# Optimization experiments

Hardware: AMD Instinct MI355X
Metric: run time of the kernel (lower is better)

## Reference

```python
import jax, jax.numpy as jnp
import numpy as np

B, H, W, C = 32, 128, 128, 64
MX, MY = 32, 32  # modes_x, modes_y


def setup_inputs() -> dict:
    key = jax.random.key(0)
    k1, k2, k3, k4 = jax.random.split(key, 4)
    # glorot-ish scales for the spectral and conv weights
    wscale = (2.0 / (C + C)) ** 0.5
    return {
        "x": jax.random.normal(k1, (B, H, W, C), dtype=jnp.float32),
        "w_real": jax.random.normal(k2, (MX, MY, C, C), dtype=jnp.float32) * wscale,
        "w_imag": jax.random.normal(k3, (MX, MY, C, C), dtype=jnp.float32) * wscale,
        "conv_w": jax.random.normal(k4, (C, C), dtype=jnp.float32) * wscale,
        "conv_b": jnp.zeros((C,), dtype=jnp.float32),
    }


def reference(x, w_real, w_imag, conv_w, conv_b):
    # Complex spectral mixing weights [MX, MY, Cin, Cout]
    weights = jax.lax.complex(w_real, w_imag)
    # tf.signal.fft2d transforms the innermost TWO axes of [B,H,W,C],
    # i.e. axes (W, C); jnp.fft.fft2 default axes=(-2,-1) matches exactly.
    x_ft = jnp.fft.fft2(x.astype(jnp.complex64))           # [B,H,W,C] complex64
    # Mode truncation on axes (H, W), as in the original code.
    x_ft_trunc = x_ft[:, :MX, :MY, :]                      # [B,MX,MY,C]
    # Complex channel-mixing einsum over the low modes.
    x_ft_proc = jnp.einsum('bxyi,xyio->bxyo', x_ft_trunc, weights)  # [B,MX,MY,C]
    # Zero-pad back to the full grid on (H, W).
    x_ft_padded = jnp.pad(x_ft_proc,
                          ((0, 0), (0, H - MX), (0, W - MY), (0, 0)))
    # IFFT again over innermost two axes (W, C), take real part.
    x_spec = jnp.real(jnp.fft.ifft2(x_ft_padded))          # [B,H,W,C] float32
    # 1x1 conv (pointwise channel mix) + bias on the raw input.
    x_local = jnp.einsum('bhwi,io->bhwo', x, conv_w) + conv_b
    return jax.nn.relu(x_spec + x_local)
```

## Files before the change

kernel.cpp:

```cpp
#include <hip/hip_runtime.h>

typedef __attribute__((ext_vector_type(8))) short short8;
typedef __attribute__((ext_vector_type(4))) float f32x4;
typedef unsigned short ushort_t;

#define MFMA(a, b, c) __builtin_amdgcn_mfma_f32_16x16x32_bf16((a), (b), (c), 0, 0, 0)

constexpr int NB = 32, NHt = 128, NWd = 128, NC = 64, MX = 32;
constexpr float TWO_PI = 6.28318530717958647692f;

constexpr size_t TAB_T1 = 0;
constexpr size_t TAB_T2 = 16384;
constexpr size_t TAB_T3 = 32768;
constexpr size_t TAB_T4 = 49152;
constexpr size_t XY_OFF = 65536;

__device__ inline ushort_t f2bf(float f) {
    union { float f; unsigned int u; } v; v.f = f;
    unsigned int r = v.u + 0x7FFFu + ((v.u >> 16) & 1u);
    return (ushort_t)(r >> 16);
}

__global__ __launch_bounds__(256) void k0_tables(ushort_t* __restrict__ tabs)
{
    int e = blockIdx.x * 256 + threadIdx.x;
    int tab = e >> 9, rem = e & 511;
    float re[8], im[8];
    if (tab == 0) {
        int mt = rem >> 8, ks = (rem >> 6) & 3, l = rem & 63;
        int uu = (l & 15) + 16 * mt, wb = (l >> 4) * 8 + 32 * ks;
        #pragma unroll
        for (int j = 0; j < 8; ++j) {
            float a = (float)((uu * (wb + j)) & 127) * (TWO_PI / 128.f);
            re[j] = cosf(a); im[j] = -sinf(a);
        }
    } else if (tab == 1) {
        int nt = rem >> 7, ks = (rem >> 6) & 1, l = rem & 63;
        int kk = (l & 15) + 16 * nt, cb2 = (l >> 4) * 8 + 32 * ks;
        #pragma unroll
        for (int j = 0; j < 8; ++j) {
            float a = (float)((kk * (cb2 + j)) & 63) * (TWO_PI / 64.f);
            re[j] = cosf(a); im[j] = -sinf(a);
        }
    } else if (tab == 2) {
        int nt = rem >> 7, ks = (rem >> 6) & 1, l = rem & 63;
        int cc = (l & 15) + 16 * nt, ob = (l >> 4) * 8 + 32 * ks;
        #pragma unroll
        for (int j = 0; j < 8; ++j) {
            float a = (float)(((ob + j) * cc) & 63) * (TWO_PI / 64.f);
            re[j] = cosf(a); im[j] = sinf(a);
        }
    } else {
        int mt = rem >> 6, l = rem & 63;
        int w = (l & 15) + 16 * mt, ub = (l >> 4) * 8;
        #pragma unroll
        for (int j = 0; j < 8; ++j) {
            float a = (float)((w * (ub + j)) & 127) * (TWO_PI / 128.f);
            re[j] = cosf(a) * 0.0001220703125f;
            im[j] = sinf(a) * 0.0001220703125f;
        }
    }
    ushort_t* dst = tabs + (size_t)e * 16;
    #pragma unroll
    for (int j = 0; j < 8; ++j) { dst[j] = f2bf(re[j]); dst[8 + j] = f2bf(im[j]); }
}

__global__ __launch_bounds__(512) void k1_fwd(
    const float* __restrict__ x, const char* __restrict__ tabs, ushort_t* __restrict__ XY)
{
    const int b = blockIdx.x, h = blockIdx.y;
    const int tid = threadIdx.x, lane = tid & 63, wv = tid >> 6;
    constexpr int SXT  = 0;
    constexpr int M1RE = 17408;
    constexpr int M1IM = 17408 + 4608;
    __shared__ __align__(16) char sm[26624];

    const float* xs = x + ((size_t)(b * NHt + h)) * (NWd * NC);
    #pragma unroll
    for (int i = 0; i < 4; ++i) {
        int idx = tid + 512 * i;
        int w = idx >> 4, c4 = (idx & 15) * 4;
        f32x4 v = *reinterpret_cast<const f32x4*>(xs + w * 64 + c4);
        #pragma unroll
        for (int j = 0; j < 4; ++j)
            *(ushort_t*)(sm + SXT + (c4 + j) * 272 + w * 2) = f2bf(v[j]);
    }
    __syncthreads();

    const int mt = wv >> 2, nt = wv & 3;
    f32x4 m1r = {0.f,0.f,0.f,0.f}, m1i = {0.f,0.f,0.f,0.f};
    #pragma unroll
    for (int ks = 0; ks < 4; ++ks) {
        short8 bfrag = *reinterpret_cast<const short8*>(
            sm + SXT + ((lane & 15) + 16 * nt) * 272 + (lane >> 4) * 16 + 64 * ks);
        const char* t1 = tabs + TAB_T1 + (((mt * 4 + ks) * 64 + lane) * 32);
        short8 are = *reinterpret_cast<const short8*>(t1);
        short8 aim = *reinterpret_cast<const short8*>(t1 + 16);
        m1r = MFMA(are, bfrag, m1r);
        m1i = MFMA(aim, bfrag, m1i);
    }
    #pragma unroll
    for (int r = 0; r < 4; ++r) {
        int u = (lane >> 4) * 4 + r + 16 * mt;
        int c = (lane & 15) + 16 * nt;
        *(ushort_t*)(sm + M1RE + u * 144 + c * 2) = f2bf(m1r[r]);
        *(ushort_t*)(sm + M1IM + u * 144 + c * 2) = f2bf(m1i[r]);
    }
    __syncthreads();

    f32x4 xP = {0.f,0.f,0.f,0.f}, xQ = {0.f,0.f,0.f,0.f}, xI = {0.f,0.f,0.f,0.f};
    #pragma unroll
    for (int ks = 0; ks < 2; ++ks) {
        short8 are = *reinterpret_cast<const short8*>(
            sm + M1RE + ((lane & 15) + 16 * mt) * 144 + (lane >> 4) * 16 + 64 * ks);
        short8 aim = *reinterpret_cast<const short8*>(
            sm + M1IM + ((lane & 15) + 16 * mt) * 144 + (lane >> 4) * 16 + 64 * ks);
        const char* t2 = tabs + TAB_T2 + (((nt * 2 + ks) * 64 + lane) * 32);
        short8 bre = *reinterpret_cast<const short8*>(t2);
        short8 bim = *reinterpret_cast<const short8*>(t2 + 16);
        xP = MFMA(are, bre, xP);
        xQ = MFMA(aim, bim, xQ);
        xI = MFMA(are, bim, xI);
        xI = MFMA(aim, bre, xI);
    }
    #pragma unroll
    for (int r = 0; r < 4; ++r) {
        int u = (lane >> 4) * 4 + r + 16 * mt;
        int k = (lane & 15) + 16 * nt;
        *(ushort_t*)(sm + SXT + 0    + u * 128 + k * 2) = f2bf(xP[r] - xQ[r]);
        *(ushort_t*)(sm + SXT + 4096 + u * 128 + k * 2) = f2bf(xI[r]);
    }
    __syncthreads();

    {
        int u = tid >> 4, comp = (tid >> 3) & 1, k8 = (tid & 7) * 8;
        short8 v = *reinterpret_cast<const short8*>(sm + SXT + comp * 4096 + u * 128 + k8 * 2);
        size_t hu = (size_t)(h * 32 + u);
        *reinterpret_cast<short8*>(XY + ((hu * 2 + comp) * 32 + b) * 64 + k8) = v;
    }
}

__global__ __launch_bounds__(256) void k2_mix(
    const float* __restrict__ wre, const float* __restrict__ wim, ushort_t* __restrict__ XY)
{
    const int h = blockIdx.x, u = blockIdx.y;
    const int tid = threadIdx.x, lane = tid & 63, wv = tid >> 6;
    constexpr int XRE = 0, XIM = 4608, WTR = 9216, WTI = 18432;
    __shared__ __align__(16) char sm[27648];
    const size_t hu = (size_t)(h * 32 + u);

    #pragma unroll
    for (int it = 0; it < 2; ++it) {
        int row = (tid >> 3) + 32 * it;
        int comp = row >> 5, bb = row & 31, k8 = (tid & 7) * 8;
        short8 v = *reinterpret_cast<const short8*>(XY + ((hu * 2 + comp) * 32 + bb) * 64 + k8);
        *reinterpret_cast<short8*>(sm + (comp ? XIM : XRE) + bb * 144 + k8 * 2) = v;
    }
    const float* wr = wre + hu * 4096;
    const float* wi = wim + hu * 4096;
    #pragma unroll
    for (int i = 0; i < 4; ++i) {
        int idx = tid + 256 * i;
        int k = idx >> 4, o4 = (idx & 15) * 4;
        f32x4 vr = __builtin_nontemporal_load(reinterpret_cast<const f32x4*>(wr + k * 64 + o4));
        f32x4 vi = __builtin_nontemporal_load(reinterpret_cast<const f32x4*>(wi + k * 64 + o4));
        #pragma unroll
        for (int j = 0; j < 4; ++j) {
            *(ushort_t*)(sm + WTR + (o4 + j) * 144 + k * 2) = f2bf(vr[j]);
            *(ushort_t*)(sm + WTI + (o4 + j) * 144 + k * 2) = f2bf(vi[j]);
        }
    }
    __syncthreads();

    const int mt = wv >> 1;
    f32x4 yRe[2], yIm[2];
    #pragma unroll
    for (int half = 0; half < 2; ++half) {
        const int nt = (wv & 1) * 2 + half;
        f32x4 yP = {0.f,0.f,0.f,0.f}, yQ = {0.f,0.f,0.f,0.f}, yI = {0.f,0.f,0.f,0.f};
        #pragma unroll
        for (int ks = 0; ks < 2; ++ks) {
            short8 are = *reinterpret_cast<const short8*>(
                sm + XRE + ((lane & 15) + 16 * mt) * 144 + (lane >> 4) * 16 + 64 * ks);
            short8 aim = *reinterpret_cast<const short8*>(
                sm + XIM + ((lane & 15) + 16 * mt) * 144 + (lane >> 4) * 16 + 64 * ks);
            short8 bre = *reinterpret_cast<const short8*>(
                sm + WTR + ((lane & 15) + 16 * nt) * 144 + (lane >> 4) * 16 + 64 * ks);
            short8 bim = *reinterpret_cast<const short8*>(
                sm + WTI + ((lane & 15) + 16 * nt) * 144 + (lane >> 4) * 16 + 64 * ks);
            yP = MFMA(are, bre, yP); yQ = MFMA(aim, bim, yQ);
            yI = MFMA(are, bim, yI); yI = MFMA(aim, bre, yI);
        }
        #pragma unroll
        for (int r = 0; r < 4; ++r) { yRe[half][r] = yP[r] - yQ[r]; yIm[half][r] = yI[r]; }
    }
    __syncthreads();

    #pragma unroll
    for (int half = 0; half < 2; ++half) {
        const int nt = (wv & 1) * 2 + half;
        #pragma unroll
        for (int r = 0; r < 4; ++r) {
            int bb = (lane >> 4) * 4 + r + 16 * mt;
            int o = (lane & 15) + 16 * nt;
            *(ushort_t*)(sm + 0    + bb * 128 + o * 2) = f2bf(yRe[half][r]);
            *(ushort_t*)(sm + 4096 + bb * 128 + o * 2) = f2bf(yIm[half][r]);
        }
    }
    __syncthreads();

    #pragma unroll
    for (int it = 0; it < 2; ++it) {
        int flat = tid + 256 * it;
        short8 v = *reinterpret_cast<const short8*>(sm + flat * 16);
        *reinterpret_cast<short8*>(XY + hu * 4096 + flat * 8) = v;
    }
}

__global__ __launch_bounds__(512) void k3_inv(
    const float* __restrict__ x, const float* __restrict__ cw, const float* __restrict__ cb,
    const char* __restrict__ tabs, const ushort_t* __restrict__ XY, float* __restrict__ out)
{
    const int b = blockIdx.x, h = blockIdx.y;
    const int tid = threadIdx.x, lane = tid & 63, wv = tid >> 6;
    constexpr int ST_RE = 0, ST_IM = 5120;
    constexpr int YRE = 10240, YIM = 14848;
    constexpr int XB  = 10240;
    constexpr int CWT = 28672;
    constexpr int SCB = 37888;
    __shared__ __align__(16) char sm[38144];

    if (h < MX) {
        {
            int u = tid >> 4, comp = (tid >> 3) & 1, o8 = (tid & 7) * 8;
            size_t hu = (size_t)(h * 32 + u);
            short8 v = *reinterpret_cast<const short8*>(XY + ((hu * 2 + comp) * 32 + b) * 64 + o8);
            *reinterpret_cast<short8*>(sm + (comp ? YIM : YRE) + u * 144 + o8 * 2) = v;
        }
        __syncthreads();
        const int mt = wv >> 2, nt = wv & 3;
        f32x4 sP = {0.f,0.f,0.f,0.f}, sQ = {0.f,0.f,0.f,0.f}, sI = {0.f,0.f,0.f,0.f};
        #pragma unroll
        for (int ks = 0; ks < 2; ++ks) {
            short8 are = *reinterpret_cast<const short8*>(
                sm + YRE + ((lane & 15) + 16 * mt) * 144 + (lane >> 4) * 16 + 64 * ks);
            short8 aim = *reinterpret_cast<const short8*>(
                sm + YIM + ((lane & 15) + 16 * mt) * 144 + (lane >> 4) * 16 + 64 * ks);
            const char* t3 = tabs + TAB_T3 + (((nt * 2 + ks) * 64 + lane) * 32);
            short8 bre = *reinterpret_cast<const short8*>(t3);
            short8 bim = *reinterpret_cast<const short8*>(t3 + 16);
            sP = MFMA(are, bre, sP); sQ = MFMA(aim, bim, sQ);
            sI = MFMA(are, bim, sI); sI = MFMA(aim, bre, sI);
        }
        #pragma unroll
        for (int r = 0; r < 4; ++r) {
            int u = (lane >> 4) * 4 + r + 16 * mt;
            int c = (lane & 15) + 16 * nt;
            *(ushort_t*)(sm + ST_RE + c * 80 + u * 2) = f2bf(sP[r] - sQ[r]);
            *(ushort_t*)(sm + ST_IM + c * 80 + u * 2) = f2bf(sI[r]);
        }
    }
    __syncthreads();

    const float* xs = x + ((size_t)(b * NHt + h)) * (NWd * NC);
    #pragma unroll
    for (int i = 0; i < 4; ++i) {
        int idx = tid + 512 * i;
        int w = idx >> 4, c4 = (idx & 15) * 4;
        f32x4 v = __builtin_nontemporal_load(reinterpret_cast<const f32x4*>(xs + w * 64 + c4));
        ushort_t h0 = f2bf(v[0]), h1 = f2bf(v[1]), h2 = f2bf(v[2]), h3 = f2bf(v[3]);
        *(unsigned int*)(sm + XB + w * 144 + c4 * 2)     = (unsigned)h0 | ((unsigned)h1 << 16);
        *(unsigned int*)(sm + XB + w * 144 + c4 * 2 + 4) = (unsigned)h2 | ((unsigned)h3 << 16);
    }
    #pragma unroll
    for (int i = 0; i < 2; ++i) {
        int ii = (tid >> 4) + 32 * i;
        #pragma unroll
        for (int j = 0; j < 4; ++j) {
            int o = (tid & 15) + 16 * j;
            *(ushort_t*)(sm + CWT + o * 144 + ii * 2) = f2bf(cw[ii * 64 + o]);
        }
    }
    if (tid < 64) ((float*)(sm + SCB))[tid] = cb[tid];
    __syncthreads();

    short8 gre = {}, gim = {};
    if (h < MX) {
        const char* t4 = tabs + TAB_T4 + ((wv * 64 + lane) * 32);
        gre = *reinterpret_cast<const short8*>(t4);
        gim = *reinterpret_cast<const short8*>(t4 + 16);
    }
    float* orow = out + ((size_t)(b * NHt + h)) * (NWd * NC);
    #pragma unroll
    for (int nt = 0; nt < 4; ++nt) {
        f32x4 acc = {0.f,0.f,0.f,0.f};
        #pragma unroll
        for (int ks = 0; ks < 2; ++ks) {
            short8 ah = *reinterpret_cast<const short8*>(
                sm + XB + ((lane & 15) + 16 * wv) * 144 + (lane >> 4) * 16 + 64 * ks);
            short8 bw = *reinterpret_cast<const short8*>(
                sm + CWT + ((lane & 15) + 16 * nt) * 144 + (lane >> 4) * 16 + 64 * ks);
            acc = MFMA(ah, bw, acc);
        }
        f32x4 sp = {0.f,0.f,0.f,0.f}, sq = {0.f,0.f,0.f,0.f};
        if (h < MX) {
            short8 bre = *reinterpret_cast<const short8*>(
                sm + ST_RE + ((lane & 15) + 16 * nt) * 80 + (lane >> 4) * 16);
            short8 bim = *reinterpret_cast<const short8*>(
                sm + ST_IM + ((lane & 15) + 16 * nt) * 80 + (lane >> 4) * 16);
            sp = MFMA(gre, bre, sp);
            sq = MFMA(gim, bim, sq);
        }
        #pragma unroll
        for (int r = 0; r < 4; ++r) {
            int w = (lane >> 4) * 4 + r + 16 * wv;
            int c = (lane & 15) + 16 * nt;
            float v = acc[r] + ((const float*)(sm + SCB))[c];
            if (h < MX) v += sp[r] - sq[r];
            orow[w * 64 + c] = fmaxf(v, 0.0f);
        }
    }
}

extern "C" void kernel_launch(void* const* d_in, const int* in_sizes, int n_in,
                              void* d_out, int out_size, void* d_ws, size_t ws_size,
                              hipStream_t stream) {
    const float* x      = (const float*)d_in[0];
    const float* w_real = (const float*)d_in[1];
    const float* w_imag = (const float*)d_in[2];
    const float* conv_w = (const float*)d_in[3];
    const float* conv_b = (const float*)d_in[4];
    float* out = (float*)d_out;

    ushort_t* tabs = (ushort_t*)d_ws;
    ushort_t* XY   = (ushort_t*)((char*)d_ws + XY_OFF);

    k0_tables<<<8, 256, 0, stream>>>(tabs);
    k1_fwd<<<dim3(NB, MX), 512, 0, stream>>>(x, (const char*)d_ws, XY);
    k2_mix<<<dim3(MX, 32), 256, 0, stream>>>(w_real, w_imag, XY);
    k3_inv<<<dim3(NB, NHt), 512, 0, stream>>>(x, conv_w, conv_b,
                                              (const char*)d_ws, XY, out);
}
```

Measured before the change: 84.56 us.

## Swizzle LDS layouts, prefetch k3 global loads early, stage output for vector stores

In the forward and mixing kernels, the transposed LDS tiles get an XOR swizzle on the column offset so the strided writes and MFMA fragment reads spread across more banks. In the inverse kernel, the x row, spectral values and twiddle fragments are loaded into registers at kernel start so their latency overlaps the spectral MFMA phase. The output is now staged in LDS and written with coalesced 16-byte nontemporal stores instead of scattered 4-byte stores. In exchange, k3 LDS use nearly doubles to about 73KB per block and launch bounds request 4 waves per SIMD, which can lower occupancy or force register spills.

```diff
diff --git a/kernel.cpp b/kernel.cpp
--- a/kernel.cpp
+++ b/kernel.cpp
@@ -1,6 +1,7 @@
 #include <hip/hip_runtime.h>
 
 typedef __attribute__((ext_vector_type(8))) short short8;
+typedef __attribute__((ext_vector_type(4))) short bf16x4;
 typedef __attribute__((ext_vector_type(4))) float f32x4;
 typedef unsigned short ushort_t;
 
@@ -20,6 +21,7 @@
     unsigned int r = v.u + 0x7FFFu + ((v.u >> 16) & 1u);
     return (ushort_t)(r >> 16);
 }
+__device__ inline int sxor(int row) { return ((row >> 3) & 3) << 4; }
 
 __global__ __launch_bounds__(256) void k0_tables(ushort_t* __restrict__ tabs)
 {
@@ -83,16 +85,17 @@
         f32x4 v = *reinterpret_cast<const f32x4*>(xs + w * 64 + c4);
         #pragma unroll
         for (int j = 0; j < 4; ++j)
-            *(ushort_t*)(sm + SXT + (c4 + j) * 272 + w * 2) = f2bf(v[j]);
+            *(ushort_t*)(sm + SXT + (c4 + j) * 272 + ((w * 2) ^ sxor(c4 + j))) = f2bf(v[j]);
     }
     __syncthreads();
 
     const int mt = wv >> 2, nt = wv & 3;
     f32x4 m1r = {0.f,0.f,0.f,0.f}, m1i = {0.f,0.f,0.f,0.f};
+    const int cc = (lane & 15) + 16 * nt;
     #pragma unroll
     for (int ks = 0; ks < 4; ++ks) {
         short8 bfrag = *reinterpret_cast<const short8*>(
-            sm + SXT + ((lane & 15) + 16 * nt) * 272 + (lane >> 4) * 16 + 64 * ks);
+            sm + SXT + cc * 272 + (((lane >> 4) * 16 + 64 * ks) ^ sxor(cc)));
         const char* t1 = tabs + TAB_T1 + (((mt * 4 + ks) * 64 + lane) * 32);
         short8 are = *reinterpret_cast<const short8*>(t1);
         short8 aim = *reinterpret_cast<const short8*>(t1 + 16);
@@ -166,8 +169,9 @@
         f32x4 vi = __builtin_nontemporal_load(reinterpret_cast<const f32x4*>(wi + k * 64 + o4));
         #pragma unroll
         for (int j = 0; j < 4; ++j) {
-            *(ushort_t*)(sm + WTR + (o4 + j) * 144 + k * 2) = f2bf(vr[j]);
-            *(ushort_t*)(sm + WTI + (o4 + j) * 144 + k * 2) = f2bf(vi[j]);
+            int o = o4 + j, koff = (k * 2) ^ sxor(o);
+            *(ushort_t*)(sm + WTR + o * 144 + koff) = f2bf(vr[j]);
+            *(ushort_t*)(sm + WTI + o * 144 + koff) = f2bf(vi[j]);
         }
     }
     __syncthreads();
@@ -177,17 +181,17 @@
     #pragma unroll
     for (int half = 0; half < 2; ++half) {
         const int nt = (wv & 1) * 2 + half;
+        const int oo = (lane & 15) + 16 * nt;
         f32x4 yP = {0.f,0.f,0.f,0.f}, yQ = {0.f,0.f,0.f,0.f}, yI = {0.f,0.f,0.f,0.f};
         #pragma unroll
         for (int ks = 0; ks < 2; ++ks) {
+            int woff = ((lane >> 4) * 16 + 64 * ks) ^ sxor(oo);
             short8 are = *reinterpret_cast<const short8*>(
                 sm + XRE + ((lane & 15) + 16 * mt) * 144 + (lane >> 4) * 16 + 64 * ks);
             short8 aim = *reinterpret_cast<const short8*>(
                 sm + XIM + ((lane & 15) + 16 * mt) * 144 + (lane >> 4) * 16 + 64 * ks);
-            short8 bre = *reinterpret_cast<const short8*>(
-                sm + WTR + ((lane & 15) + 16 * nt) * 144 + (lane >> 4) * 16 + 64 * ks);
-            short8 bim = *reinterpret_cast<const short8*>(
-                sm + WTI + ((lane & 15) + 16 * nt) * 144 + (lane >> 4) * 16 + 64 * ks);
+            short8 bre = *reinterpret_cast<const short8*>(sm + WTR + oo * 144 + woff);
+            short8 bim = *reinterpret_cast<const short8*>(sm + WTI + oo * 144 + woff);
             yP = MFMA(are, bre, yP); yQ = MFMA(aim, bim, yQ);
             yI = MFMA(are, bim, yI); yI = MFMA(aim, bre, yI);
         }
@@ -217,25 +221,62 @@
     }
 }
 
-__global__ __launch_bounds__(512) void k3_inv(
+__global__ __launch_bounds__(512, 4) void k3_inv(
     const float* __restrict__ x, const float* __restrict__ cw, const float* __restrict__ cb,
     const char* __restrict__ tabs, const ushort_t* __restrict__ XY, float* __restrict__ out)
 {
     const int b = blockIdx.x, h = blockIdx.y;
     const int tid = threadIdx.x, lane = tid & 63, wv = tid >> 6;
     constexpr int ST_RE = 0, ST_IM = 5120;
-    constexpr int YRE = 10240, YIM = 14848;
-    constexpr int XB  = 10240;
-    constexpr int CWT = 28672;
-    constexpr int SCB = 37888;
-    __shared__ __align__(16) char sm[38144];
+    constexpr int XB   = 10240;
+    constexpr int CWT  = 28672;
+    constexpr int SCB  = 37888;
+    constexpr int OUTB = 38144;
+    constexpr int YRE  = 38144;
+    constexpr int YIM  = 38144 + 4608;
+    __shared__ __align__(16) char sm[72960];
+
+    const float* xs = x + ((size_t)(b * NHt + h)) * (NWd * NC);
+    f32x4 xv[4];
+    #pragma unroll
+    for (int i = 0; i < 4; ++i) {
+        int idx = tid + 512 * i;
+        int w = idx >> 4, c4 = (idx & 15) * 4;
+        xv[i] = __builtin_nontemporal_load(reinterpret_cast<const f32x4*>(xs + w * 64 + c4));
+    }
+    short8 yv = {}, gre = {}, gim = {};
+    if (h < MX) {
+        int u = tid >> 4, comp = (tid >> 3) & 1, o8 = (tid & 7) * 8;
+        size_t hu = (size_t)(h * 32 + u);
+        yv = *reinterpret_cast<const short8*>(XY + ((hu * 2 + comp) * 32 + b) * 64 + o8);
+        const char* t4 = tabs + TAB_T4 + ((wv * 64 + lane) * 32);
+        gre = *reinterpret_cast<const short8*>(t4);
+        gim = *reinterpret_cast<const short8*>(t4 + 16);
+    }
+
+    #pragma unroll
+    for (int i = 0; i < 4; ++i) {
+        int idx = tid + 512 * i;
+        int w = idx >> 4, c4 = (idx & 15) * 4;
+        bf16x4 pk = { (short)f2bf(xv[i][0]), (short)f2bf(xv[i][1]),
+                      (short)f2bf(xv[i][2]), (short)f2bf(xv[i][3]) };
+        *reinterpret_cast<bf16x4*>(sm + XB + w * 144 + c4 * 2) = pk;
+    }
+    #pragma unroll
+    for (int i = 0; i < 2; ++i) {
+        int ii = (tid >> 4) + 32 * i;
+        #pragma unroll
+        for (int j = 0; j < 4; ++j) {
+            int o = (tid & 15) + 16 * j;
+            *(ushort_t*)(sm + CWT + o * 144 + ii * 2) = f2bf(cw[ii * 64 + o]);
+        }
+    }
+    if (tid < 64) ((float*)(sm + SCB))[tid] = cb[tid];
 
     if (h < MX) {
         {
             int u = tid >> 4, comp = (tid >> 3) & 1, o8 = (tid & 7) * 8;
-            size_t hu = (size_t)(h * 32 + u);
-            short8 v = *reinterpret_cast<const short8*>(XY + ((hu * 2 + comp) * 32 + b) * 64 + o8);
-            *reinterpret_cast<short8*>(sm + (comp ? YIM : YRE) + u * 144 + o8 * 2) = v;
+            *reinterpret_cast<short8*>(sm + (comp ? YIM : YRE) + u * 144 + o8 * 2) = yv;
         }
         __syncthreads();
         const int mt = wv >> 2, nt = wv & 3;
@@ -262,35 +303,6 @@
     }
     __syncthreads();
 
-    const float* xs = x + ((size_t)(b * NHt + h)) * (NWd * NC);
-    #pragma unroll
-    for (int i = 0; i < 4; ++i) {
-        int idx = tid + 512 * i;
-        int w = idx >> 4, c4 = (idx & 15) * 4;
-        f32x4 v = __builtin_nontemporal_load(reinterpret_cast<const f32x4*>(xs + w * 64 + c4));
-        ushort_t h0 = f2bf(v[0]), h1 = f2bf(v[1]), h2 = f2bf(v[2]), h3 = f2bf(v[3]);
-        *(unsigned int*)(sm + XB + w * 144 + c4 * 2)     = (unsigned)h0 | ((unsigned)h1 << 16);
-        *(unsigned int*)(sm + XB + w * 144 + c4 * 2 + 4) = (unsigned)h2 | ((unsigned)h3 << 16);
-    }
-    #pragma unroll
-    for (int i = 0; i < 2; ++i) {
-        int ii = (tid >> 4) + 32 * i;
-        #pragma unroll
-        for (int j = 0; j < 4; ++j) {
-            int o = (tid & 15) + 16 * j;
-            *(ushort_t*)(sm + CWT + o * 144 + ii * 2) = f2bf(cw[ii * 64 + o]);
-        }
-    }
-    if (tid < 64) ((float*)(sm + SCB))[tid] = cb[tid];
-    __syncthreads();
-
-    short8 gre = {}, gim = {};
-    if (h < MX) {
-        const char* t4 = tabs + TAB_T4 + ((wv * 64 + lane) * 32);
-        gre = *reinterpret_cast<const short8*>(t4);
-        gim = *reinterpret_cast<const short8*>(t4 + 16);
-    }
-    float* orow = out + ((size_t)(b * NHt + h)) * (NWd * NC);
     #pragma unroll
     for (int nt = 0; nt < 4; ++nt) {
         f32x4 acc = {0.f,0.f,0.f,0.f};
@@ -317,8 +329,18 @@
             int c = (lane & 15) + 16 * nt;
             float v = acc[r] + ((const float*)(sm + SCB))[c];
             if (h < MX) v += sp[r] - sq[r];
-            orow[w * 64 + c] = fmaxf(v, 0.0f);
-        }
+            *(float*)(sm + OUTB + w * 272 + c * 4) = fmaxf(v, 0.0f);
+        }
+    }
+    __syncthreads();
+
+    float* orow = out + ((size_t)(b * NHt + h)) * (NWd * NC);
+    #pragma unroll
+    for (int i = 0; i < 4; ++i) {
+        int flat = tid + 512 * i;
+        int w = flat >> 4, c4 = (flat & 15) * 4;
+        f32x4 v = *reinterpret_cast<const f32x4*>(sm + OUTB + w * 272 + c4 * 4);
+        __builtin_nontemporal_store(v, reinterpret_cast<f32x4*>(orow + w * 64 + c4));
     }
 }
 
```

Measured after the change: 83.91 us. No clear change (-0.8%).
